# Optimization experiments

Hardware: AMD Instinct MI355X
Metric: run time of the kernel (lower is better)

## Reference

```python
import jax, jax.numpy as jnp
from jax import lax
import numpy as np

B, T = 256, 100
N_FEAT, V, E, H = 64, 32, 8, 512
CAT_POS = np.arange(0, N_FEAT, 4)                                 # 16 categorical feature indices
CONT_POS = np.array([k for k in range(N_FEAT) if k % 4 != 0])      # 48 continuous feature indices
N_CAT, N_CONT = len(CAT_POS), len(CONT_POS)
IN_LEN = N_FEAT + N_CAT * (E - 1)                                  # 176, matches input_linear.in_features
N_LAYERS = 2                                                        # len(hidden_layers) - 1 LSTMs

# Precompute the interleaved output layout of embed(): walking feature index k,
# categorical features occupy E slots, continuous features 1 slot.
def _layout():
    cont_off, cat_off, cur = [], [], 0
    for k in range(N_FEAT):
        if k % 4 == 0:
            cat_off.append(cur); cur += E
        else:
            cont_off.append(cur); cur += 1
    return np.array(cont_off), np.array(cat_off)
CONT_OFF, CAT_OFF = _layout()
CAT_COLS = (CAT_OFF[:, None] + np.arange(E)).ravel()               # [N_CAT*E] target columns


def lstm(x, Wih, Whh, bih, bhh):
    # PyTorch LSTM, batch_first, gate order (i, f, g, o).
    xw = jnp.einsum('bti,gi->btg', x, Wih) + bih                   # [B,T,4H] input projection (one GEMM)
    def step(carry, xw_t):
        h, c = carry
        gates = xw_t + h @ Whh.T + bhh
        i, f, g, o = jnp.split(gates, 4, axis=-1)
        c = jax.nn.sigmoid(f) * c + jax.nn.sigmoid(i) * jnp.tanh(g)
        h = jax.nn.sigmoid(o) * jnp.tanh(c)
        return (h, c), h
    h0 = jnp.zeros((x.shape[0], Whh.shape[1]), x.dtype)
    (_, _), hs = lax.scan(step, (h0, h0), jnp.swapaxes(xw, 0, 1))
    return jnp.swapaxes(hs, 0, 1)                                   # [B,T,H]


def setup_inputs() -> dict:
    key = jax.random.key(0)
    ks = jax.random.split(key, 16)
    s = 0.05
    base = jax.random.normal(ks[0], (B, T, N_FEAT), jnp.float32)
    cats = jax.random.randint(ks[1], (B, T, N_CAT), 0, V)
    x = base.at[..., CAT_POS].set(cats.astype(jnp.float32))
    return {
        'x': x,
        'scaler_mean': jax.random.normal(ks[2], (N_FEAT,), jnp.float32),
        'scaler_scale': jax.random.uniform(ks[3], (N_FEAT,), jnp.float32, minval=0.5, maxval=2.0),
        'emb': jax.random.normal(ks[4], (N_CAT, V, E), jnp.float32) * s,
        'W_in': jax.random.normal(ks[5], (IN_LEN, H), jnp.float32) * s,
        'b_in': jnp.zeros((H,), jnp.float32),
        'Wih': jax.random.normal(ks[6], (N_LAYERS, 4 * H, H), jnp.float32) * s,
        'Whh': jax.random.normal(ks[7], (N_LAYERS, 4 * H, H), jnp.float32) * s,
        'bih': jnp.zeros((N_LAYERS, 4 * H), jnp.float32),
        'bhh': jnp.zeros((N_LAYERS, 4 * H), jnp.float32),
        'W_out': jax.random.normal(ks[8], (H, N_CONT), jnp.float32) * s,
        'b_out': jnp.zeros((N_CONT,), jnp.float32),
        'W_cls': jax.random.normal(ks[9], (N_CAT, H, V), jnp.float32) * s,
        'b_cls': jnp.zeros((N_CAT, V), jnp.float32),
    }


def reference(x, scaler_mean, scaler_scale, emb, W_in, b_in, Wih, Whh, bih, bhh, W_out, b_out, W_cls, b_cls):
    # ---- embed(): vectorized replacement of the triple python loop ----
    scaled = (x - scaler_mean) / scaler_scale                      # sklearn StandardScaler.transform
    cont_vals = scaled[..., CONT_POS]                              # [B,T,48]
    idx = x[..., CAT_POS].astype(jnp.int32)                        # [B,T,16] categorical codes
    embv = emb[jnp.arange(N_CAT)[None, None, :], idx]              # [B,T,16,E] gather
    new = jnp.zeros((x.shape[0], x.shape[1], IN_LEN), x.dtype)
    new = new.at[..., CONT_OFF].set(cont_vals)
    new = new.at[..., CAT_COLS].set(embv.reshape(x.shape[0], x.shape[1], N_CAT * E))
    # ---- input linear + activation ----
    h = jax.nn.relu(new @ W_in + b_in)                             # [B,T,512]
    # ---- stacked LSTMs, activation after each ----
    for l in range(N_LAYERS):
        h = jax.nn.relu(lstm(h, Wih[l], Whh[l], bih[l], bhh[l]))
    last = h[:, -1, :]                                             # [B,512]
    cont_out = last @ W_out + b_out                                # [B,48]
    cls_out = jnp.einsum('bh,nhv->bnv', last, W_cls) + b_cls       # [B,16,32] classification heads
    return (cont_out, cls_out)
```

## Files before the change

### kernel.cpp

```cpp
#include <hip/hip_runtime.h>

#define BB 256
#define TT 100
#define HH 512
#define G4 2048
#define INL 176
#define KIN 192
#define NCAT 16
#define NCONT 48
#define VV 32
#define EE 8
#define MTOT (BB*TT)
#define GRPB 32
#define FS 16

typedef unsigned short u16;
typedef unsigned int   u32;
typedef unsigned long long u64;
typedef __attribute__((ext_vector_type(8))) short bf16x8;
typedef __attribute__((ext_vector_type(4))) float f32x4;

__device__ __forceinline__ float bf2f(u16 u){
    union { u32 i; float f; } v; v.i = ((u32)u) << 16; return v.f;
}
__device__ __forceinline__ u16 f2bf(float f){
    union { float f; u32 i; } v; v.f = f;
    u32 b = v.i;
    b += 0x7FFFu + ((b >> 16) & 1u);
    return (u16)(b >> 16);
}
__device__ __forceinline__ float fast_tanh(float x){
    float e = __expf(2.f * x);
    return 1.f - 2.f / (e + 1.f);
}
__device__ __forceinline__ u64 relu4_bf16(u64 v){
    u64 s = v & 0x8000800080008000ULL;
    u64 m = s - (s >> 15);
    return v & ~(s | m);
}

__global__ void PredictionModel_58841051955204_kernel(
    const float* __restrict__ Win, u16* __restrict__ WinT){
    int idx = blockIdx.x*256 + threadIdx.x;
    if (idx >= HH*KIN) return;
    int h = idx / KIN, i = idx % KIN;
    WinT[idx] = (i < INL) ? f2bf(Win[i*HH + h]) : (u16)0;
}

__global__ void k_cvt(const float* __restrict__ in, u16* __restrict__ out, int n){
    int i = blockIdx.x*256 + threadIdx.x;
    if (i < n) out[i] = f2bf(in[i]);
}

__global__ void k_feat(const float* __restrict__ x, const float* __restrict__ mean,
                       const float* __restrict__ scale, const float* __restrict__ emb,
                       u16* __restrict__ feat){
    int idx = blockIdx.x*256 + threadIdx.x;
    int bt = idx >> 4, g = idx & 15;
    if (bt >= MTOT) return;
    const float* xr = x + (size_t)bt*64;
    u16* fr = feat + (size_t)bt*KIN;
    int k0 = g*4;
    int ci = (int)xr[k0];
    if (ci < 0) ci = 0;
    if (ci > VV-1) ci = VV-1;
    const float* ep = emb + (size_t)(g*VV + ci)*EE;
    int c0 = g*11;
    for (int e = 0; e < 8; e++) fr[c0+e] = f2bf(ep[e]);
    for (int j = 1; j <= 3; j++){
        int k = k0 + j;
        fr[c0 + 8 + (j-1)] = f2bf((xr[k] - mean[k]) / scale[k]);
    }
    fr[INL + g] = 0;
}

__global__ __launch_bounds__(256) void k_gemm(
    const u16* __restrict__ A, int lda,
    const u16* __restrict__ W, int K,
    const float* __restrict__ bias1, const float* __restrict__ bias2,
    void* __restrict__ out, int ldo, int kc_cnt, int do_relu, int out_half)
{
    __shared__ u16 sA[64*40];
    __shared__ u16 sB[256*40];
    int tid = threadIdx.x;
    int w = tid >> 6, lane = tid & 63, q = lane >> 4, r = lane & 15;
    int m0 = blockIdx.x * 64;
    int n0 = blockIdx.y * 256;

    f32x4 acc[4][4];
    for (int a_ = 0; a_ < 4; a_++)
        for (int b_ = 0; b_ < 4; b_++){
            acc[a_][b_][0] = 0.f; acc[a_][b_][1] = 0.f;
            acc[a_][b_][2] = 0.f; acc[a_][b_][3] = 0.f;
        }

    for (int kc = 0; kc < kc_cnt; kc++){
        {
            int row = tid >> 2, seg = tid & 3;
            uint4 v = *(const uint4*)(A + (size_t)(m0+row)*lda + kc*32 + seg*8);
            *(uint4*)(&sA[row*40 + seg*8]) = v;
            const u16* wr = W + (size_t)(n0 + tid)*K + kc*32;
            uint4 b0 = *(const uint4*)(wr);
            uint4 b1 = *(const uint4*)(wr+8);
            uint4 b2 = *(const uint4*)(wr+16);
            uint4 b3 = *(const uint4*)(wr+24);
            u16* d = &sB[tid*40];
            *(uint4*)(d)    = b0; *(uint4*)(d+8)  = b1;
            *(uint4*)(d+16) = b2; *(uint4*)(d+24) = b3;
        }
        __syncthreads();
        bf16x8 a[4], b[4];
        for (int mt = 0; mt < 4; mt++) a[mt] = *(const bf16x8*)(&sA[(mt*16 + r)*40 + q*8]);
        for (int i = 0; i < 4; i++)    b[i]  = *(const bf16x8*)(&sB[((w*4+i)*16 + r)*40 + q*8]);
        for (int mt = 0; mt < 4; mt++)
            for (int i = 0; i < 4; i++)
                acc[mt][i] = __builtin_amdgcn_mfma_f32_16x16x32_bf16(a[mt], b[i], acc[mt][i], 0, 0, 0);
        __syncthreads();
    }

    for (int i = 0; i < 4; i++){
        int n = n0 + (w*4+i)*16 + r;
        float bs = 0.f;
        if (bias1) bs += bias1[n];
        if (bias2) bs += bias2[n];
        for (int mt = 0; mt < 4; mt++){
            for (int reg = 0; reg < 4; reg++){
                int m = m0 + mt*16 + q*4 + reg;
                float v = acc[mt][i][reg] + bs;
                if (do_relu) v = fmaxf(v, 0.f);
                if (out_half) ((_Float16*)out)[(size_t)m*ldo + n] = (_Float16)v;
                else          ((u16*)out)[(size_t)m*ldo + n] = f2bf(v);
            }
        }
    }
}

__global__ void k_zcnt(int* bar){
    int i = blockIdx.x*256 + threadIdx.x;
    if (i < 4096)
        __hip_atomic_store(&bar[i], 0, __ATOMIC_RELAXED, __HIP_MEMORY_SCOPE_AGENT);
}

__global__ __launch_bounds__(256, 1) void k_rec2(
    const u16* __restrict__ Whhb,
    const u16* __restrict__ Wihb1,
    const _Float16* __restrict__ xw,
    const float* __restrict__ bih, const float* __restrict__ bhh,
    u64* __restrict__ h0r,
    u64* __restrict__ h1A, u64* __restrict__ h1B,
    int* __restrict__ bar)
{
    extern __shared__ u16 smem[];
    int tid = threadIdx.x;
    int w = tid >> 6, lane = tid & 63, q = lane >> 4, r = lane & 15;
    int lay  = blockIdx.x >> 7;
    int bid7 = blockIdx.x & 127;
    int mg = bid7 & 3, jb = bid7 >> 2;
    int m0 = mg*64, j0 = jb*16;
    int j = j0 + r;
    int* F0x = bar;
    int* F1x = bar + 2048;
    int fidx = (mg*GRPB + jb)*FS;

    {
        int row = tid >> 2, seg = tid & 3;
        int g = row >> 4, jj = row & 15;
        const u16* srcW = Whhb + (size_t)lay*G4*HH + (size_t)(g*HH + j0 + jj)*HH;
        u16* sW = smem + (lay ? 64*512 : 0);
        for (int i = 0; i < 16; i++){
            int c = seg*16 + i;
            *(uint4*)(&sW[row*512 + ((c ^ (row & 7)) * 8)]) = *(const uint4*)(srcW + c*8);
        }
        if (lay){
            const u16* srcI = Wihb1 + (size_t)(g*HH + j0 + jj)*HH;
            for (int i = 0; i < 16; i++){
                int c = seg*16 + i;
                *(uint4*)(&smem[row*512 + ((c ^ (row & 7)) * 8)]) = *(const uint4*)(srcI + c*8);
            }
        }
    }
    float creg[4] = {0.f, 0.f, 0.f, 0.f};
    if (!lay && (r & 3) == 0){
        u64* hz = h0r + (size_t)3*BB*(HH/4);
        for (int reg = 0; reg < 4; reg++){
            int m = m0 + w*16 + q*4 + reg;
            __hip_atomic_store(&hz[(size_t)m*(HH/4) + ((j0 + r) >> 2)], 0ULL,
                               __ATOMIC_RELAXED, __HIP_MEMORY_SCOPE_AGENT);
        }
    }
    asm volatile("s_waitcnt vmcnt(0)" ::: "memory");
    __syncthreads();
    if (tid == 0)
        __hip_atomic_store(lay ? &F1x[fidx] : &F0x[fidx], 1,
                           __ATOMIC_RELAXED, __HIP_MEMORY_SCOPE_AGENT);
    if (tid < GRPB){
        int* fp = (lay ? F1x : F0x) + (mg*GRPB + tid)*FS;
        long long t0c = clock64();
        while (__hip_atomic_load(fp, __ATOMIC_RELAXED, __HIP_MEMORY_SCOPE_AGENT) < 1){
            __builtin_amdgcn_s_sleep(1);
            if (clock64() - t0c > 50000000LL) break;
        }
    }
    __syncthreads();

    if (!lay){
        float xnxt[4][4];
        #pragma unroll
        for (int reg = 0; reg < 4; reg++){
            int m = m0 + w*16 + q*4 + reg;
            const _Float16* xr = xw + ((size_t)m*TT + 0)*G4 + j;
            #pragma unroll
            for (int g = 0; g < 4; g++)
                xnxt[reg][g] = (float)__builtin_nontemporal_load(xr + g*HH);
        }

        for (int t = 0; t < TT; t++){
            const u64* hsrc = h0r + (size_t)((t + 3) & 3)*BB*(HH/4);
            u32* hdst32 = (u32*)(h0r + (size_t)(t & 3)*BB*(HH/4));
            const u64* hrow = hsrc + (size_t)(m0 + w*16 + r)*(HH/4);

            float xcur[4][4];
            #pragma unroll
            for (int reg = 0; reg < 4; reg++)
                #pragma unroll
                for (int g = 0; g < 4; g++)
                    xcur[reg][g] = xnxt[reg][g];

            u64 hd[32];
            #pragma unroll
            for (int kc = 0; kc < 16; kc++){
                int jg0 = kc*8 + q*2;
                hd[kc*2]   = __hip_atomic_load(&hrow[jg0],   __ATOMIC_RELAXED, __HIP_MEMORY_SCOPE_AGENT);
                hd[kc*2+1] = __hip_atomic_load(&hrow[jg0+1], __ATOMIC_RELAXED, __HIP_MEMORY_SCOPE_AGENT);
            }
            if (t + 1 < TT){
                #pragma unroll
                for (int reg = 0; reg < 4; reg++){
                    int m = m0 + w*16 + q*4 + reg;
                    const _Float16* xr = xw + ((size_t)m*TT + (t+1))*G4 + j;
                    #pragma unroll
                    for (int g = 0; g < 4; g++)
                        xnxt[reg][g] = (float)__builtin_nontemporal_load(xr + g*HH);
                }
            }
            asm volatile("" :
                "+v"(hd[0]),  "+v"(hd[1]),  "+v"(hd[2]),  "+v"(hd[3]),
                "+v"(hd[4]),  "+v"(hd[5]),  "+v"(hd[6]),  "+v"(hd[7]),
                "+v"(hd[8]),  "+v"(hd[9]),  "+v"(hd[10]), "+v"(hd[11]),
                "+v"(hd[12]), "+v"(hd[13]), "+v"(hd[14]), "+v"(hd[15]));
            asm volatile("" :
                "+v"(hd[16]), "+v"(hd[17]), "+v"(hd[18]), "+v"(hd[19]),
                "+v"(hd[20]), "+v"(hd[21]), "+v"(hd[22]), "+v"(hd[23]),
                "+v"(hd[24]), "+v"(hd[25]), "+v"(hd[26]), "+v"(hd[27]),
                "+v"(hd[28]), "+v"(hd[29]), "+v"(hd[30]), "+v"(hd[31]));
            __builtin_amdgcn_sched_barrier(0);

            f32x4 acc[4];
            for (int g = 0; g < 4; g++){
                acc[g][0] = 0.f; acc[g][1] = 0.f; acc[g][2] = 0.f; acc[g][3] = 0.f;
            }
            #pragma unroll
            for (int kc = 0; kc < 16; kc++){
                union { u64 d[2]; bf16x8 v; } au;
                au.d[0] = hd[kc*2];
                au.d[1] = hd[kc*2+1];
                int cbase = kc*4 + q;
                #pragma unroll
                for (int g = 0; g < 4; g++){
                    int row = g*16 + r;
                    bf16x8 b = *(const bf16x8*)(&smem[row*512 + ((cbase ^ (row & 7)) * 8)]);
                    acc[g] = __builtin_amdgcn_mfma_f32_16x16x32_bf16(au.v, b, acc[g], 0, 0, 0);
                }
            }

            #pragma unroll
            for (int reg = 0; reg < 4; reg++){
                int m = m0 + w*16 + q*4 + reg;
                float Gi = acc[0][reg] + xcur[reg][0];
                float Gf = acc[1][reg] + xcur[reg][1];
                float Gg = acc[2][reg] + xcur[reg][2];
                float Go = acc[3][reg] + xcur[reg][3];
                float iv = 1.f/(1.f + __expf(-Gi));
                float fv = 1.f/(1.f + __expf(-Gf));
                float gv = fast_tanh(Gg);
                float ov = 1.f/(1.f + __expf(-Go));
                float c = fv * creg[reg] + iv * gv;
                creg[reg] = c;
                float h = ov * fast_tanh(c);
                u32 own = (u32)f2bf(h);
                u32 p01 = own | (((u32)__shfl_xor((int)own, 1)) << 16);
                if ((r & 1) == 0){
                    __hip_atomic_store(&hdst32[(size_t)m*(HH/2) + ((j0 + r) >> 1)], p01,
                                       __ATOMIC_RELAXED, __HIP_MEMORY_SCOPE_AGENT);
                }
            }

            asm volatile("s_waitcnt vmcnt(0)" ::: "memory");
            __syncthreads();
            if (tid == 0)
                __hip_atomic_store(&F0x[fidx], t + 2, __ATOMIC_RELAXED, __HIP_MEMORY_SCOPE_AGENT);
            if (t + 1 < TT){
                if (tid < 64){
                    long long t0c = clock64();
                    const int* fp; int thr;
                    if (lane < GRPB){ fp = &F0x[(mg*GRPB + lane)*FS];        thr = t + 2; }
                    else            { fp = &F1x[(mg*GRPB + (lane-GRPB))*FS]; thr = t - 1; }
                    while (__hip_atomic_load(fp, __ATOMIC_RELAXED, __HIP_MEMORY_SCOPE_AGENT) < thr){
                        __builtin_amdgcn_s_sleep(1);
                        if (clock64() - t0c > 50000000LL) break;
                    }
                }
                __syncthreads();
            }
        }
    } else {
        const u16* sWih = smem;
        const u16* sWhh = smem + 64*512;
        float bs1[4];
        for (int g = 0; g < 4; g++)
            bs1[g] = bih[G4 + g*HH + j] + bhh[G4 + g*HH + j];

        if (tid < GRPB){
            const int* fp = &F0x[(mg*GRPB + tid)*FS];
            long long t0c = clock64();
            while (__hip_atomic_load(fp, __ATOMIC_RELAXED, __HIP_MEMORY_SCOPE_AGENT) < 2){
                __builtin_amdgcn_s_sleep(1);
                if (clock64() - t0c > 50000000LL) break;
            }
        }
        __syncthreads();

        f32x4 acc_hh[4];
        for (int g = 0; g < 4; g++){
            acc_hh[g][0] = 0.f; acc_hh[g][1] = 0.f; acc_hh[g][2] = 0.f; acc_hh[g][3] = 0.f;
        }

        for (int t = 0; t < TT; t++){
            const u64* xsrc = h0r + (size_t)(t & 3)*BB*(HH/4);
            u64*       hdst = (t & 1) ? h1A : h1B;
            const u64* xrow = xsrc + (size_t)(m0 + w*16 + r)*(HH/4);

            u64 hx[32];
            #pragma unroll
            for (int kc = 0; kc < 16; kc++){
                int jg0 = kc*8 + q*2;
                hx[kc*2]   = relu4_bf16(__hip_atomic_load(&xrow[jg0],   __ATOMIC_RELAXED, __HIP_MEMORY_SCOPE_AGENT));
                hx[kc*2+1] = relu4_bf16(__hip_atomic_load(&xrow[jg0+1], __ATOMIC_RELAXED, __HIP_MEMORY_SCOPE_AGENT));
            }
            asm volatile("" :
                "+v"(hx[0]),  "+v"(hx[1]),  "+v"(hx[2]),  "+v"(hx[3]),
                "+v"(hx[4]),  "+v"(hx[5]),  "+v"(hx[6]),  "+v"(hx[7]),
                "+v"(hx[8]),  "+v"(hx[9]),  "+v"(hx[10]), "+v"(hx[11]),
                "+v"(hx[12]), "+v"(hx[13]), "+v"(hx[14]), "+v"(hx[15]));
            asm volatile("" :
                "+v"(hx[16]), "+v"(hx[17]), "+v"(hx[18]), "+v"(hx[19]),
                "+v"(hx[20]), "+v"(hx[21]), "+v"(hx[22]), "+v"(hx[23]),
                "+v"(hx[24]), "+v"(hx[25]), "+v"(hx[26]), "+v"(hx[27]),
                "+v"(hx[28]), "+v"(hx[29]), "+v"(hx[30]), "+v"(hx[31]));
            __builtin_amdgcn_sched_barrier(0);

            f32x4 acc[4];
            for (int g = 0; g < 4; g++) acc[g] = acc_hh[g];
            #pragma unroll
            for (int kc = 0; kc < 16; kc++){
                union { u64 d[2]; bf16x8 v; } au;
                au.d[0] = hx[kc*2];
                au.d[1] = hx[kc*2+1];
                int cbase = kc*4 + q;
                #pragma unroll
                for (int g = 0; g < 4; g++){
                    int row = g*16 + r;
                    bf16x8 b = *(const bf16x8*)(&sWih[row*512 + ((cbase ^ (row & 7)) * 8)]);
                    acc[g] = __builtin_amdgcn_mfma_f32_16x16x32_bf16(au.v, b, acc[g], 0, 0, 0);
                }
            }

            u32* hdst32 = (u32*)hdst;
            #pragma unroll
            for (int reg = 0; reg < 4; reg++){
                int m = m0 + w*16 + q*4 + reg;
                float Gi = acc[0][reg] + bs1[0];
                float Gf = acc[1][reg] + bs1[1];
                float Gg = acc[2][reg] + bs1[2];
                float Go = acc[3][reg] + bs1[3];
                float iv = 1.f/(1.f + __expf(-Gi));
                float fv = 1.f/(1.f + __expf(-Gf));
                float gv = fast_tanh(Gg);
                float ov = 1.f/(1.f + __expf(-Go));
                float c = fv * creg[reg] + iv * gv;
                creg[reg] = c;
                float h = ov * fast_tanh(c);
                u32 own = (u32)f2bf(h);
                u32 p01 = own | (((u32)__shfl_xor((int)own, 1)) << 16);
                if ((r & 1) == 0){
                    __hip_atomic_store(&hdst32[(size_t)m*(HH/2) + ((j0 + r) >> 1)], p01,
                                       __ATOMIC_RELAXED, __HIP_MEMORY_SCOPE_AGENT);
                }
            }

            asm volatile("s_waitcnt vmcnt(0)" ::: "memory");
            __syncthreads();
            if (tid == 0)
                __hip_atomic_store(&F1x[fidx], t + 2, __ATOMIC_RELAXED, __HIP_MEMORY_SCOPE_AGENT);

            if (t + 1 < TT){
                if (tid < GRPB){
                    const int* fp = &F1x[(mg*GRPB + tid)*FS];
                    long long t0c = clock64();
                    while (__hip_atomic_load(fp, __ATOMIC_RELAXED, __HIP_MEMORY_SCOPE_AGENT) < t + 2){
                        __builtin_amdgcn_s_sleep(1);
                        if (clock64() - t0c > 50000000LL) break;
                    }
                }
                __syncthreads();

                const u64* hrow = hdst + (size_t)(m0 + w*16 + r)*(HH/4);
                u64 hh[32];
                #pragma unroll
                for (int kc = 0; kc < 16; kc++){
                    int jg0 = kc*8 + q*2;
                    hh[kc*2]   = __hip_atomic_load(&hrow[jg0],   __ATOMIC_RELAXED, __HIP_MEMORY_SCOPE_AGENT);
                    hh[kc*2+1] = __hip_atomic_load(&hrow[jg0+1], __ATOMIC_RELAXED, __HIP_MEMORY_SCOPE_AGENT);
                }
                asm volatile("" :
                    "+v"(hh[0]),  "+v"(hh[1]),  "+v"(hh[2]),  "+v"(hh[3]),
                    "+v"(hh[4]),  "+v"(hh[5]),  "+v"(hh[6]),  "+v"(hh[7]),
                    "+v"(hh[8]),  "+v"(hh[9]),  "+v"(hh[10]), "+v"(hh[11]),
                    "+v"(hh[12]), "+v"(hh[13]), "+v"(hh[14]), "+v"(hh[15]));
                asm volatile("" :
                    "+v"(hh[16]), "+v"(hh[17]), "+v"(hh[18]), "+v"(hh[19]),
                    "+v"(hh[20]), "+v"(hh[21]), "+v"(hh[22]), "+v"(hh[23]),
                    "+v"(hh[24]), "+v"(hh[25]), "+v"(hh[26]), "+v"(hh[27]),
                    "+v"(hh[28]), "+v"(hh[29]), "+v"(hh[30]), "+v"(hh[31]));
                __builtin_amdgcn_sched_barrier(0);

                for (int g = 0; g < 4; g++){
                    acc_hh[g][0] = 0.f; acc_hh[g][1] = 0.f;
                    acc_hh[g][2] = 0.f; acc_hh[g][3] = 0.f;
                }
                #pragma unroll
                for (int kc = 0; kc < 16; kc++){
                    union { u64 d[2]; bf16x8 v; } au;
                    au.d[0] = hh[kc*2];
                    au.d[1] = hh[kc*2+1];
                    int cbase = kc*4 + q;
                    #pragma unroll
                    for (int g = 0; g < 4; g++){
                        int row = g*16 + r;
                        bf16x8 b = *(const bf16x8*)(&sWhh[row*512 + ((cbase ^ (row & 7)) * 8)]);
                        acc_hh[g] = __builtin_amdgcn_mfma_f32_16x16x32_bf16(au.v, b, acc_hh[g], 0, 0, 0);
                    }
                }

                if (tid < GRPB){
                    const int* fp = &F0x[(mg*GRPB + tid)*FS];
                    long long t0c = clock64();
                    while (__hip_atomic_load(fp, __ATOMIC_RELAXED, __HIP_MEMORY_SCOPE_AGENT) < t + 3){
                        __builtin_amdgcn_s_sleep(1);
                        if (clock64() - t0c > 50000000LL) break;
                    }
                }
                __syncthreads();
            }
        }
    }
}

__global__ void k_heads(
    const u16* __restrict__ hfin, const float* __restrict__ Wout,
    const float* __restrict__ bout, const float* __restrict__ Wcls,
    const float* __restrict__ bcls, float* __restrict__ out)
{
    __shared__ float last[HH];
    int b = blockIdx.x, tid = threadIdx.x;
    for (int h = tid; h < HH; h += 256) last[h] = fmaxf(bf2f(hfin[b*HH + h]), 0.f);
    __syncthreads();
    for (int o = tid; o < NCONT + NCAT*VV; o += 256){
        if (o < NCONT){
            float a = bout[o];
            for (int h = 0; h < HH; h++) a += last[h] * Wout[h*NCONT + o];
            out[b*NCONT + o] = (a == 0.0f) ? 7.0f : a;
        } else {
            int oc = o - NCONT;
            int n = oc >> 5, v = oc & 31;
            float a = bcls[oc];
            const float* wp = Wcls + (size_t)n*HH*VV + v;
            for (int h = 0; h < HH; h++) a += last[h] * wp[h*VV];
            out[BB*NCONT + b*(NCAT*VV) + oc] = (a == 0.0f) ? 7.0f : a;
        }
    }
}

extern "C" void kernel_launch(void* const* d_in, const int* in_sizes, int n_in,
                              void* d_out, int out_size, void* d_ws, size_t ws_size,
                              hipStream_t stream){
    const float* x      = (const float*)d_in[0];
    const float* smean  = (const float*)d_in[1];
    const float* sscale = (const float*)d_in[2];
    const float* emb    = (const float*)d_in[3];
    const float* Win    = (const float*)d_in[4];
    const float* bin    = (const float*)d_in[5];
    const float* Wih    = (const float*)d_in[6];
    const float* Whh    = (const float*)d_in[7];
    const float* bih    = (const float*)d_in[8];
    const float* bhh    = (const float*)d_in[9];
    const float* Wout   = (const float*)d_in[10];
    const float* bout   = (const float*)d_in[11];
    const float* Wcls   = (const float*)d_in[12];
    const float* bcls   = (const float*)d_in[13];
    (void)in_sizes; (void)n_in; (void)out_size;

    char* ws = (char*)d_ws;
    size_t off = 0;
    u16*      feat  = (u16*)(ws + off);      off += (size_t)MTOT*KIN*2;
    u16*      WinTb = (u16*)(ws + off);      off += (size_t)HH*KIN*2;
    u16*      Xbuf  = (u16*)(ws + off);      off += (size_t)MTOT*HH*2;
    _Float16* xw    = (_Float16*)(ws + off); off += (size_t)MTOT*G4*2;
    u16*      Wihb  = (u16*)(ws + off);      off += (size_t)2*G4*HH*2;
    u16*      Whhb  = (u16*)(ws + off);      off += (size_t)2*G4*HH*2;
    u64*      h0r   = (u64*)(ws + off);      off += (size_t)4*BB*HH*2;
    u64*      h1A   = (u64*)(ws + off);      off += (size_t)BB*HH*2;
    u64*      h1B   = (u64*)(ws + off);      off += (size_t)BB*HH*2;
    int*      bar   = (int*)(ws + off);      off += 4096*4;
    (void)off; (void)ws_size;

    PredictionModel_58841051955204_kernel<<<384, 256, 0, stream>>>(Win, WinTb);
    k_cvt<<<8192, 256, 0, stream>>>(Wih, Wihb, 2*G4*HH);
    k_cvt<<<8192, 256, 0, stream>>>(Whh, Whhb, 2*G4*HH);

    k_feat<<<1600, 256, 0, stream>>>(x, smean, sscale, emb, feat);
    k_gemm<<<dim3(400, 2), 256, 0, stream>>>(feat, KIN, WinTb, KIN, bin, (const float*)0,
                                             Xbuf, HH, 6, 1, 0);
    k_gemm<<<dim3(400, 8), 256, 0, stream>>>(Xbuf, HH, Wihb, HH, bih, bhh,
                                             xw, G4, 16, 0, 1);
    k_zcnt<<<16, 256, 0, stream>>>(bar);
    k_rec2<<<256, 256, 131072, stream>>>(Whhb, Wihb + (size_t)G4*HH, xw, bih, bhh,
                                         h0r, h1A, h1B, bar);
    k_heads<<<256, 256, 0, stream>>>((const u16*)h1A, Wout, bout, Wcls, bcls, (float*)d_out);
}
```

Measured before the change: 1.535 ms.

## Fuse layer-0 input projection into recurrent kernel and simplify layer-1 step

Drops the separate xw GEMM that precomputed the layer-0 input projection into an fp16 [B*T,2048] buffer. Layer 0 now keeps Wih in LDS and does the Xbuf·Wih product with MFMA inside each timestep, prefetching the next step's Xbuf row. Layer 1 now reads its own previous h at the start of each step and waits once for both flags, instead of running the Whh product early between two separate waits. This saves a large GEMM and the xw memory traffic, but doubles the MFMA work on the serial path of layer 0 and serialises layer 1's hh load behind its wait.

```diff
diff --git a/kernel.cpp b/kernel.cpp
--- a/kernel.cpp
+++ b/kernel.cpp
@@ -142,9 +142,9 @@
 }
 
 __global__ __launch_bounds__(256, 1) void k_rec2(
+    const u16* __restrict__ Wihb,
     const u16* __restrict__ Whhb,
-    const u16* __restrict__ Wihb1,
-    const _Float16* __restrict__ xw,
+    const u16* __restrict__ Xbuf,
     const float* __restrict__ bih, const float* __restrict__ bhh,
     u64* __restrict__ h0r,
     u64* __restrict__ h1A, u64* __restrict__ h1B,
@@ -161,27 +161,23 @@
     int* F0x = bar;
     int* F1x = bar + 2048;
     int fidx = (mg*GRPB + jb)*FS;
+    const u16* sWih = smem;
+    const u16* sWhh = smem + 64*512;
 
     {
         int row = tid >> 2, seg = tid & 3;
         int g = row >> 4, jj = row & 15;
+        const u16* srcI = Wihb + (size_t)lay*G4*HH + (size_t)(g*HH + j0 + jj)*HH;
         const u16* srcW = Whhb + (size_t)lay*G4*HH + (size_t)(g*HH + j0 + jj)*HH;
-        u16* sW = smem + (lay ? 64*512 : 0);
         for (int i = 0; i < 16; i++){
             int c = seg*16 + i;
-            *(uint4*)(&sW[row*512 + ((c ^ (row & 7)) * 8)]) = *(const uint4*)(srcW + c*8);
-        }
-        if (lay){
-            const u16* srcI = Wihb1 + (size_t)(g*HH + j0 + jj)*HH;
-            for (int i = 0; i < 16; i++){
-                int c = seg*16 + i;
-                *(uint4*)(&smem[row*512 + ((c ^ (row & 7)) * 8)]) = *(const uint4*)(srcI + c*8);
-            }
+            *(uint4*)(&smem[row*512 + ((c ^ (row & 7)) * 8)]) = *(const uint4*)(srcI + c*8);
+            *(uint4*)(&smem[64*512 + row*512 + ((c ^ (row & 7)) * 8)]) = *(const uint4*)(srcW + c*8);
         }
     }
     float creg[4] = {0.f, 0.f, 0.f, 0.f};
-    if (!lay && (r & 3) == 0){
-        u64* hz = h0r + (size_t)3*BB*(HH/4);
+    if ((r & 3) == 0){
+        u64* hz = lay ? h1A : (h0r + (size_t)3*BB*(HH/4));
         for (int reg = 0; reg < 4; reg++){
             int m = m0 + w*16 + q*4 + reg;
             __hip_atomic_store(&hz[(size_t)m*(HH/4) + ((j0 + r) >> 2)], 0ULL,
@@ -203,15 +199,21 @@
     }
     __syncthreads();
 
+    float bs[4];
+    for (int g = 0; g < 4; g++)
+        bs[g] = bih[lay*G4 + g*HH + j] + bhh[lay*G4 + g*HH + j];
+
     if (!lay){
-        float xnxt[4][4];
-        #pragma unroll
-        for (int reg = 0; reg < 4; reg++){
-            int m = m0 + w*16 + q*4 + reg;
-            const _Float16* xr = xw + ((size_t)m*TT + 0)*G4 + j;
-            #pragma unroll
-            for (int g = 0; g < 4; g++)
-                xnxt[reg][g] = (float)__builtin_nontemporal_load(xr + g*HH);
+        const u64* xb = (const u64*)Xbuf;
+        u64 xn[32];
+        {
+            const u64* xrow = xb + ((size_t)(m0 + w*16 + r)*TT + 0)*(HH/4);
+            #pragma unroll
+            for (int kc = 0; kc < 16; kc++){
+                int jg0 = kc*8 + q*2;
+                xn[kc*2]   = __builtin_nontemporal_load(&xrow[jg0]);
+                xn[kc*2+1] = __builtin_nontemporal_load(&xrow[jg0+1]);
+            }
         }
 
         for (int t = 0; t < TT; t++){
@@ -219,29 +221,12 @@
             u32* hdst32 = (u32*)(h0r + (size_t)(t & 3)*BB*(HH/4));
             const u64* hrow = hsrc + (size_t)(m0 + w*16 + r)*(HH/4);
 
-            float xcur[4][4];
-            #pragma unroll
-            for (int reg = 0; reg < 4; reg++)
-                #pragma unroll
-                for (int g = 0; g < 4; g++)
-                    xcur[reg][g] = xnxt[reg][g];
-
             u64 hd[32];
             #pragma unroll
             for (int kc = 0; kc < 16; kc++){
                 int jg0 = kc*8 + q*2;
                 hd[kc*2]   = __hip_atomic_load(&hrow[jg0],   __ATOMIC_RELAXED, __HIP_MEMORY_SCOPE_AGENT);
                 hd[kc*2+1] = __hip_atomic_load(&hrow[jg0+1], __ATOMIC_RELAXED, __HIP_MEMORY_SCOPE_AGENT);
-            }
-            if (t + 1 < TT){
-                #pragma unroll
-                for (int reg = 0; reg < 4; reg++){
-                    int m = m0 + w*16 + q*4 + reg;
-                    const _Float16* xr = xw + ((size_t)m*TT + (t+1))*G4 + j;
-                    #pragma unroll
-                    for (int g = 0; g < 4; g++)
-                        xnxt[reg][g] = (float)__builtin_nontemporal_load(xr + g*HH);
-                }
             }
             asm volatile("" :
                 "+v"(hd[0]),  "+v"(hd[1]),  "+v"(hd[2]),  "+v"(hd[3]),
@@ -262,24 +247,46 @@
             #pragma unroll
             for (int kc = 0; kc < 16; kc++){
                 union { u64 d[2]; bf16x8 v; } au;
+                au.d[0] = xn[kc*2];
+                au.d[1] = xn[kc*2+1];
+                int cbase = kc*4 + q;
+                #pragma unroll
+                for (int g = 0; g < 4; g++){
+                    int row = g*16 + r;
+                    bf16x8 b = *(const bf16x8*)(&sWih[row*512 + ((cbase ^ (row & 7)) * 8)]);
+                    acc[g] = __builtin_amdgcn_mfma_f32_16x16x32_bf16(au.v, b, acc[g], 0, 0, 0);
+                }
+            }
+            #pragma unroll
+            for (int kc = 0; kc < 16; kc++){
+                union { u64 d[2]; bf16x8 v; } au;
                 au.d[0] = hd[kc*2];
                 au.d[1] = hd[kc*2+1];
                 int cbase = kc*4 + q;
                 #pragma unroll
                 for (int g = 0; g < 4; g++){
                     int row = g*16 + r;
-                    bf16x8 b = *(const bf16x8*)(&smem[row*512 + ((cbase ^ (row & 7)) * 8)]);
+                    bf16x8 b = *(const bf16x8*)(&sWhh[row*512 + ((cbase ^ (row & 7)) * 8)]);
                     acc[g] = __builtin_amdgcn_mfma_f32_16x16x32_bf16(au.v, b, acc[g], 0, 0, 0);
+                }
+            }
+            if (t + 1 < TT){
+                const u64* xrow = xb + ((size_t)(m0 + w*16 + r)*TT + (t+1))*(HH/4);
+                #pragma unroll
+                for (int kc = 0; kc < 16; kc++){
+                    int jg0 = kc*8 + q*2;
+                    xn[kc*2]   = __builtin_nontemporal_load(&xrow[jg0]);
+                    xn[kc*2+1] = __builtin_nontemporal_load(&xrow[jg0+1]);
                 }
             }
 
             #pragma unroll
             for (int reg = 0; reg < 4; reg++){
                 int m = m0 + w*16 + q*4 + reg;
-                float Gi = acc[0][reg] + xcur[reg][0];
-                float Gf = acc[1][reg] + xcur[reg][1];
-                float Gg = acc[2][reg] + xcur[reg][2];
-                float Go = acc[3][reg] + xcur[reg][3];
+                float Gi = acc[0][reg] + bs[0];
+                float Gf = acc[1][reg] + bs[1];
+                float Gg = acc[2][reg] + bs[2];
+                float Go = acc[3][reg] + bs[3];
                 float iv = 1.f/(1.f + __expf(-Gi));
                 float fv = 1.f/(1.f + __expf(-Gf));
                 float gv = fast_tanh(Gg);
@@ -314,12 +321,6 @@
             }
         }
     } else {
-        const u16* sWih = smem;
-        const u16* sWhh = smem + 64*512;
-        float bs1[4];
-        for (int g = 0; g < 4; g++)
-            bs1[g] = bih[G4 + g*HH + j] + bhh[G4 + g*HH + j];
-
         if (tid < GRPB){
             const int* fp = &F0x[(mg*GRPB + tid)*FS];
             long long t0c = clock64();
@@ -330,22 +331,25 @@
         }
         __syncthreads();
 
-        f32x4 acc_hh[4];
-        for (int g = 0; g < 4; g++){
-            acc_hh[g][0] = 0.f; acc_hh[g][1] = 0.f; acc_hh[g][2] = 0.f; acc_hh[g][3] = 0.f;
-        }
-
         for (int t = 0; t < TT; t++){
             const u64* xsrc = h0r + (size_t)(t & 3)*BB*(HH/4);
+            const u64* hsrc = (t & 1) ? h1B : h1A;
             u64*       hdst = (t & 1) ? h1A : h1B;
             const u64* xrow = xsrc + (size_t)(m0 + w*16 + r)*(HH/4);
-
-            u64 hx[32];
+            const u64* hrow = hsrc + (size_t)(m0 + w*16 + r)*(HH/4);
+
+            u64 hx[32], hh[32];
             #pragma unroll
             for (int kc = 0; kc < 16; kc++){
                 int jg0 = kc*8 + q*2;
                 hx[kc*2]   = relu4_bf16(__hip_atomic_load(&xrow[jg0],   __ATOMIC_RELAXED, __HIP_MEMORY_SCOPE_AGENT));
                 hx[kc*2+1] = relu4_bf16(__hip_atomic_load(&xrow[jg0+1], __ATOMIC_RELAXED, __HIP_MEMORY_SCOPE_AGENT));
+            }
+            #pragma unroll
+            for (int kc = 0; kc < 16; kc++){
+                int jg0 = kc*8 + q*2;
+                hh[kc*2]   = __hip_atomic_load(&hrow[jg0],   __ATOMIC_RELAXED, __HIP_MEMORY_SCOPE_AGENT);
+                hh[kc*2+1] = __hip_atomic_load(&hrow[jg0+1], __ATOMIC_RELAXED, __HIP_MEMORY_SCOPE_AGENT);
             }
             asm volatile("" :
                 "+v"(hx[0]),  "+v"(hx[1]),  "+v"(hx[2]),  "+v"(hx[3]),
@@ -357,10 +361,22 @@
                 "+v"(hx[20]), "+v"(hx[21]), "+v"(hx[22]), "+v"(hx[23]),
                 "+v"(hx[24]), "+v"(hx[25]), "+v"(hx[26]), "+v"(hx[27]),
                 "+v"(hx[28]), "+v"(hx[29]), "+v"(hx[30]), "+v"(hx[31]));
+            asm volatile("" :
+                "+v"(hh[0]),  "+v"(hh[1]),  "+v"(hh[2]),  "+v"(hh[3]),
+                "+v"(hh[4]),  "+v"(hh[5]),  "+v"(hh[6]),  "+v"(hh[7]),
+                "+v"(hh[8]),  "+v"(hh[9]),  "+v"(hh[10]), "+v"(hh[11]),
+                "+v"(hh[12]), "+v"(hh[13]), "+v"(hh[14]), "+v"(hh[15]));
+            asm volatile("" :
+                "+v"(hh[16]), "+v"(hh[17]), "+v"(hh[18]), "+v"(hh[19]),
+                "+v"(hh[20]), "+v"(hh[21]), "+v"(hh[22]), "+v"(hh[23]),
+                "+v"(hh[24]), "+v"(hh[25]), "+v"(hh[26]), "+v"(hh[27]),
+                "+v"(hh[28]), "+v"(hh[29]), "+v"(hh[30]), "+v"(hh[31]));
             __builtin_amdgcn_sched_barrier(0);
 
             f32x4 acc[4];
-            for (int g = 0; g < 4; g++) acc[g] = acc_hh[g];
+            for (int g = 0; g < 4; g++){
+                acc[g][0] = 0.f; acc[g][1] = 0.f; acc[g][2] = 0.f; acc[g][3] = 0.f;
+            }
             #pragma unroll
             for (int kc = 0; kc < 16; kc++){
                 union { u64 d[2]; bf16x8 v; } au;
@@ -374,15 +390,28 @@
                     acc[g] = __builtin_amdgcn_mfma_f32_16x16x32_bf16(au.v, b, acc[g], 0, 0, 0);
                 }
             }
+            #pragma unroll
+            for (int kc = 0; kc < 16; kc++){
+                union { u64 d[2]; bf16x8 v; } au;
+                au.d[0] = hh[kc*2];
+                au.d[1] = hh[kc*2+1];
+                int cbase = kc*4 + q;
+                #pragma unroll
+                for (int g = 0; g < 4; g++){
+                    int row = g*16 + r;
+                    bf16x8 b = *(const bf16x8*)(&sWhh[row*512 + ((cbase ^ (row & 7)) * 8)]);
+                    acc[g] = __builtin_amdgcn_mfma_f32_16x16x32_bf16(au.v, b, acc[g], 0, 0, 0);
+                }
+            }
 
             u32* hdst32 = (u32*)hdst;
             #pragma unroll
             for (int reg = 0; reg < 4; reg++){
                 int m = m0 + w*16 + q*4 + reg;
-                float Gi = acc[0][reg] + bs1[0];
-                float Gf = acc[1][reg] + bs1[1];
-                float Gg = acc[2][reg] + bs1[2];
-                float Go = acc[3][reg] + bs1[3];
+                float Gi = acc[0][reg] + bs[0];
+                float Gf = acc[1][reg] + bs[1];
+                float Gg = acc[2][reg] + bs[2];
+                float Go = acc[3][reg] + bs[3];
                 float iv = 1.f/(1.f + __expf(-Gi));
                 float fv = 1.f/(1.f + __expf(-Gf));
                 float gv = fast_tanh(Gg);
@@ -404,58 +433,12 @@
                 __hip_atomic_store(&F1x[fidx], t + 2, __ATOMIC_RELAXED, __HIP_MEMORY_SCOPE_AGENT);
 
             if (t + 1 < TT){
-                if (tid < GRPB){
-                    const int* fp = &F1x[(mg*GRPB + tid)*FS];
+                if (tid < 64){
                     long long t0c = clock64();
-                    while (__hip_atomic_load(fp, __ATOMIC_RELAXED, __HIP_MEMORY_SCOPE_AGENT) < t + 2){
-                        __builtin_amdgcn_s_sleep(1);
-                        if (clock64() - t0c > 50000000LL) break;
-                    }
-                }
-                __syncthreads();
-
-                const u64* hrow = hdst + (size_t)(m0 + w*16 + r)*(HH/4);
-                u64 hh[32];
-                #pragma unroll
-                for (int kc = 0; kc < 16; kc++){
-                    int jg0 = kc*8 + q*2;
-                    hh[kc*2]   = __hip_atomic_load(&hrow[jg0],   __ATOMIC_RELAXED, __HIP_MEMORY_SCOPE_AGENT);
-                    hh[kc*2+1] = __hip_atomic_load(&hrow[jg0+1], __ATOMIC_RELAXED, __HIP_MEMORY_SCOPE_AGENT);
-                }
-                asm volatile("" :
-                    "+v"(hh[0]),  "+v"(hh[1]),  "+v"(hh[2]),  "+v"(hh[3]),
-                    "+v"(hh[4]),  "+v"(hh[5]),  "+v"(hh[6]),  "+v"(hh[7]),
-                    "+v"(hh[8]),  "+v"(hh[9]),  "+v"(hh[10]), "+v"(hh[11]),
-                    "+v"(hh[12]), "+v"(hh[13]), "+v"(hh[14]), "+v"(hh[15]));
-                asm volatile("" :
-                    "+v"(hh[16]), "+v"(hh[17]), "+v"(hh[18]), "+v"(hh[19]),
-                    "+v"(hh[20]), "+v"(hh[21]), "+v"(hh[22]), "+v"(hh[23]),
-                    "+v"(hh[24]), "+v"(hh[25]), "+v"(hh[26]), "+v"(hh[27]),
-                    "+v"(hh[28]), "+v"(hh[29]), "+v"(hh[30]), "+v"(hh[31]));
-                __builtin_amdgcn_sched_barrier(0);
-
-                for (int g = 0; g < 4; g++){
-                    acc_hh[g][0] = 0.f; acc_hh[g][1] = 0.f;
-                    acc_hh[g][2] = 0.f; acc_hh[g][3] = 0.f;
-                }
-                #pragma unroll
-                for (int kc = 0; kc < 16; kc++){
-                    union { u64 d[2]; bf16x8 v; } au;
-                    au.d[0] = hh[kc*2];
-                    au.d[1] = hh[kc*2+1];
-                    int cbase = kc*4 + q;
-                    #pragma unroll
-                    for (int g = 0; g < 4; g++){
-                        int row = g*16 + r;
-                        bf16x8 b = *(const bf16x8*)(&sWhh[row*512 + ((cbase ^ (row & 7)) * 8)]);
-                        acc_hh[g] = __builtin_amdgcn_mfma_f32_16x16x32_bf16(au.v, b, acc_hh[g], 0, 0, 0);
-                    }
-                }
-
-                if (tid < GRPB){
-                    const int* fp = &F0x[(mg*GRPB + tid)*FS];
-                    long long t0c = clock64();
-                    while (__hip_atomic_load(fp, __ATOMIC_RELAXED, __HIP_MEMORY_SCOPE_AGENT) < t + 3){
+                    const int* fp; int thr;
+                    if (lane < GRPB){ fp = &F1x[(mg*GRPB + lane)*FS];        thr = t + 2; }
+                    else            { fp = &F0x[(mg*GRPB + (lane-GRPB))*FS]; thr = t + 3; }
+                    while (__hip_atomic_load(fp, __ATOMIC_RELAXED, __HIP_MEMORY_SCOPE_AGENT) < thr){
                         __builtin_amdgcn_s_sleep(1);
                         if (clock64() - t0c > 50000000LL) break;
                     }
@@ -515,7 +498,6 @@
     u16*      feat  = (u16*)(ws + off);      off += (size_t)MTOT*KIN*2;
     u16*      WinTb = (u16*)(ws + off);      off += (size_t)HH*KIN*2;
     u16*      Xbuf  = (u16*)(ws + off);      off += (size_t)MTOT*HH*2;
-    _Float16* xw    = (_Float16*)(ws + off); off += (size_t)MTOT*G4*2;
     u16*      Wihb  = (u16*)(ws + off);      off += (size_t)2*G4*HH*2;
     u16*      Whhb  = (u16*)(ws + off);      off += (size_t)2*G4*HH*2;
     u64*      h0r   = (u64*)(ws + off);      off += (size_t)4*BB*HH*2;
@@ -531,10 +513,8 @@
     k_feat<<<1600, 256, 0, stream>>>(x, smean, sscale, emb, feat);
     k_gemm<<<dim3(400, 2), 256, 0, stream>>>(feat, KIN, WinTb, KIN, bin, (const float*)0,
                                              Xbuf, HH, 6, 1, 0);
-    k_gemm<<<dim3(400, 8), 256, 0, stream>>>(Xbuf, HH, Wihb, HH, bih, bhh,
-                                             xw, G4, 16, 0, 1);
     k_zcnt<<<16, 256, 0, stream>>>(bar);
-    k_rec2<<<256, 256, 131072, stream>>>(Whhb, Wihb + (size_t)G4*HH, xw, bih, bhh,
+    k_rec2<<<256, 256, 131072, stream>>>(Wihb, Whhb, Xbuf, bih, bhh,
                                          h0r, h1A, h1B, bar);
     k_heads<<<256, 256, 0, stream>>>((const u16*)h1A, Wout, bout, Wcls, bcls, (float*)d_out);
 }
```

Result: faster. 1.351 ms (-12.0%).
